# Kernel optimization log

Hardware: AMD Instinct MI355X
Metric: run time of the kernel (lower is better)

The kernel has to match this reference:

```python
import jax, jax.numpy as jnp
from jax import lax
import numpy as np

D, DI, S, K, R = 128, 256, 16, 4, 8  # d_model, d_inner, d_state, d_conv, dt_rank
B, W, N, E = 8, 64, 128, 256


def _ln(x, g, b, eps=1e-5):
    m = x.mean(-1, keepdims=True)
    v = ((x - m) ** 2).mean(-1, keepdims=True)
    return (x - m) * lax.rsqrt(v + eps) * g + b


def _mamba(x, w_in, conv_w, conv_b, w_xp, dt_w, dt_b, Alog, Dp, w_out):
    # x: (Bq, W, D) -> (Bq, W, D). Faithful mamba_ssm.Mamba math (selective scan).
    Bq, Wlen, _ = x.shape
    xz = x @ w_in                       # (Bq, W, 2*DI)
    xc, z = jnp.split(xz, 2, axis=-1)
    # causal depthwise conv over time
    xt = xc.transpose(0, 2, 1)          # (Bq, DI, W)
    xt = lax.conv_general_dilated(xt, conv_w[:, None, :], (1,), [(K - 1, 0)],
                                  feature_group_count=DI)
    xc = jax.nn.silu(xt + conv_b[None, :, None]).transpose(0, 2, 1)  # (Bq, W, DI)
    dbc = xc @ w_xp                     # (Bq, W, R+2S)
    dt = jax.nn.softplus(dbc[..., :R] @ dt_w + dt_b)   # (Bq, W, DI)
    Bm = dbc[..., R:R + S]              # (Bq, W, S)
    Cm = dbc[..., R + S:]               # (Bq, W, S)
    A = -jnp.exp(Alog)                  # (DI, S)

    def step(h, inp):
        dt_t, B_t, C_t, x_t = inp       # (Bq,DI),(Bq,S),(Bq,S),(Bq,DI)
        dA = jnp.exp(dt_t[..., None] * A)                 # (Bq,DI,S)
        h = dA * h + (dt_t * x_t)[..., None] * B_t[:, None, :]
        y = jnp.einsum('bds,bs->bd', h, C_t)
        return h, y

    h0 = jnp.zeros((Bq, DI, S), x.dtype)
    _, ys = lax.scan(step, h0, (dt.transpose(1, 0, 2), Bm.transpose(1, 0, 2),
                                Cm.transpose(1, 0, 2), xc.transpose(1, 0, 2)))
    y = ys.transpose(1, 0, 2) + xc * Dp          # D skip connection
    y = y * jax.nn.silu(z)
    return y @ w_out


def _forward(x_node, x_trace, x_log, mp_in, mp_conv_w, mp_conv_b, mp_xproj,
             mp_dt_w, mp_dt_b, mp_Alog, mp_D, mp_out, mix_w, mix_b,
             an_g, an_b, ff1_w, ff1_b, ff2_w, ff2_b, fln_g, fln_b):
    Bz, Wz, Nz, _ = x_node.shape
    Ez = x_trace.shape[2]
    # (B,W,N,D) -> (B*N, W, D) per-entity temporal sequences
    sn = x_node.transpose(0, 2, 1, 3).reshape(Bz * Nz, Wz, D)
    st = x_trace.transpose(0, 2, 1, 3).reshape(Bz * Ez, Wz, D)
    sl = x_log.transpose(0, 2, 1, 3).reshape(Bz * Nz, Wz, D)

    def mam(i, s):
        return _mamba(s, mp_in[i], mp_conv_w[i], mp_conv_b[i], mp_xproj[i],
                      mp_dt_w[i], mp_dt_b[i], mp_Alog[i], mp_D[i], mp_out[i])

    yn, yt, yl = mam(0, sn), mam(1, st), mam(2, sl)

    # cross-modal mixing of node & log with residual (dropout = identity in eval)
    cat = jnp.concatenate([yn, yl], axis=-1)          # (B*N, W, 2D)
    cat = cat + jax.nn.silu(cat @ mix_w + mix_b)
    yn, yl = jnp.split(cat, 2, axis=-1)

    # back to (B, W, N/E, D)
    yn = yn.reshape(Bz, Nz, Wz, D).transpose(0, 2, 1, 3)
    yt = yt.reshape(Bz, Ez, Wz, D).transpose(0, 2, 1, 3)
    yl = yl.reshape(Bz, Nz, Wz, D).transpose(0, 2, 1, 3)

    # AddALL: AddNorm(old, new) = LN(dropout(new) + old)
    n1 = _ln(yn + x_node, an_g[0], an_b[0])
    t1 = _ln(yt + x_trace, an_g[1], an_b[1])
    l1 = _ln(yl + x_log, an_g[2], an_b[2])

    # FFN: AddNorm(x, FeedForward(x)) per modality, LeakyReLU(0.01)
    def ffn(i, x):
        h = jax.nn.leaky_relu(x @ ff1_w[i] + ff1_b[i], 0.01)
        return _ln(h @ ff2_w[i] + ff2_b[i] + x, fln_g[i], fln_b[i])

    n2, t2, l2 = ffn(0, n1), ffn(1, t1), ffn(2, l1)
    # concat along entity axis (all feature dims = D) for a single output
    return jnp.concatenate([n2, t2, l2], axis=2)      # (B, W, 2N+E, D)


def setup_inputs() -> dict:
    key = jax.random.key(0)
    ks = jax.random.split(key, 16)
    f = lambda k, shp, s=1.0: jax.random.normal(k, shp, dtype=jnp.float32) * s
    return {
        'x_node': f(ks[0], (B, W, N, D)),
        'x_trace': f(ks[1], (B, W, E, D)),
        'x_log': f(ks[2], (B, W, N, D)),
        'mp_in': f(ks[3], (3, D, 2 * DI), 0.05),
        'mp_conv_w': f(ks[4], (3, DI, K), 0.2),
        'mp_conv_b': jnp.zeros((3, DI), jnp.float32),
        'mp_xproj': f(ks[5], (3, DI, R + 2 * S), 0.05),
        'mp_dt_w': f(ks[6], (3, R, DI), 0.1),
        'mp_dt_b': jnp.full((3, DI), float(np.log(np.expm1(0.01))), jnp.float32),
        'mp_Alog': jnp.log(jnp.broadcast_to(jnp.arange(1, S + 1, dtype=jnp.float32), (3, DI, S))),
        'mp_D': jnp.ones((3, DI), jnp.float32),
        'mp_out': f(ks[7], (3, DI, D), 0.05),
        'mix_w': f(ks[8], (2 * D, 2 * D), 0.05),
        'mix_b': jnp.zeros((2 * D,), jnp.float32),
        'an_g': jnp.ones((3, D), jnp.float32),
        'an_b': jnp.zeros((3, D), jnp.float32),
        'ff1_w': f(ks[9], (3, D, 4 * D), 0.05),
        'ff1_b': jnp.zeros((3, 4 * D), jnp.float32),
        'ff2_w': f(ks[10], (3, 4 * D, D), 0.05),
        'ff2_b': jnp.zeros((3, D), jnp.float32),
        'fln_g': jnp.ones((3, D), jnp.float32),
        'fln_b': jnp.zeros((3, D), jnp.float32),
    }


def reference(x_node, x_trace, x_log, mp_in, mp_conv_w, mp_conv_b, mp_xproj,
              mp_dt_w, mp_dt_b, mp_Alog, mp_D, mp_out, mix_w, mix_b,
              an_g, an_b, ff1_w, ff1_b, ff2_w, ff2_b, fln_g, fln_b):
    return _forward(x_node, x_trace, x_log, mp_in, mp_conv_w, mp_conv_b,
                    mp_xproj, mp_dt_w, mp_dt_b, mp_Alog, mp_D, mp_out,
                    mix_w, mix_b, an_g, an_b, ff1_w, ff1_b, ff2_w, ff2_b,
                    fln_g, fln_b)
```

## Files before the change

### kernel.cpp

```cpp
#include <hip/hip_runtime.h>
#include <hip/hip_bf16.h>

#define DEV __device__ __forceinline__

typedef __attribute__((ext_vector_type(8))) short bf16x8;
typedef __attribute__((ext_vector_type(4))) float f32x4;
typedef __attribute__((ext_vector_type(2))) float f32x2;

DEV f32x4 MF(bf16x8 a, bf16x8 b, f32x4 c) {
  return __builtin_amdgcn_mfma_f32_16x16x32_bf16(a, b, c, 0, 0, 0);
}

DEV float bf2f(unsigned short u) {
  union { unsigned int i; float f; } v; v.i = ((unsigned int)u) << 16; return v.f;
}
DEV unsigned short f2bf(float f) {
  __hip_bfloat16 h = __float2bfloat16(f);
  unsigned short r; __builtin_memcpy(&r, &h, 2); return r;
}
DEV unsigned int packbf(float a, float b) {
  float2 p; p.x = a; p.y = b;
  __hip_bfloat162 h = __float22bfloat162_rn(p);
  unsigned int r; __builtin_memcpy(&r, &h, 4); return r;
}
#define LOG2E 1.442695041f
#define LN2   0.6931471806f
DEV float silu_fast(float v) {
  float e = __builtin_amdgcn_exp2f(v * -LOG2E);
  return v * __builtin_amdgcn_rcpf(1.f + e);
}
DEV float softplus_fast(float v) {
  float e = __builtin_amdgcn_exp2f(v * LOG2E);
  float l = __builtin_amdgcn_logf(1.f + e) * LN2;
  return v > 15.f ? v : l;
}

#define WS_WINT   0
#define WS_WXPT   196608
#define WS_WOUTT  233472
#define WS_FF1T   331776
#define WS_FF2T   528384
#define WS_MIXT   724992
#define WS_TOTAL  790528

__global__ __launch_bounds__(256) void prep_kernel(
    const float* __restrict__ w_in, const float* __restrict__ w_xp,
    const float* __restrict__ w_out, const float* __restrict__ ff1,
    const float* __restrict__ ff2, const float* __restrict__ mixw,
    unsigned short* __restrict__ ws)
{
  int idx = blockIdx.x * 256 + threadIdx.x;
  if (idx >= WS_TOTAL) return;
  float v;
  if (idx < WS_WXPT) {
    int j = idx, s = j / 65536, r = j % 65536, n = r >> 7, k = r & 127;
    v = w_in[s * 65536 + k * 512 + n];
  } else if (idx < WS_WOUTT) {
    int j = idx - WS_WXPT, s = j / 12288, r = j % 12288, n = r >> 8, k = r & 255;
    v = (n < 40) ? w_xp[s * 10240 + k * 40 + n] : 0.f;
  } else if (idx < WS_FF1T) {
    int j = idx - WS_WOUTT, s = j / 32768, r = j % 32768, n = r >> 8, k = r & 255;
    v = w_out[s * 32768 + k * 128 + n];
  } else if (idx < WS_FF2T) {
    int j = idx - WS_FF1T, s = j / 65536, r = j % 65536, n = r >> 7, k = r & 127;
    v = ff1[s * 65536 + k * 512 + n];
  } else if (idx < WS_MIXT) {
    int j = idx - WS_FF2T, s = j / 65536, r = j % 65536, n = r >> 9, k = r & 511;
    v = ff2[s * 65536 + k * 128 + n];
  } else {
    int j = idx - WS_MIXT, n = j >> 8, k = j & 255;
    v = mixw[k * 256 + n];
  }
  ws[idx] = f2bf(v);
}

__global__ __launch_bounds__(256, 2) void mamba_front(
    const float* __restrict__ xn, const float* __restrict__ xt,
    const float* __restrict__ xl,
    const unsigned short* __restrict__ w_inT_all,
    const float* __restrict__ conv_w_all, const float* __restrict__ conv_b_all,
    const unsigned short* __restrict__ w_xpT_all,
    const float* __restrict__ dt_w_all, const float* __restrict__ dt_b_all,
    const float* __restrict__ Alog_all, const float* __restrict__ Dp_all,
    const unsigned short* __restrict__ w_outT_all,
    const float* __restrict__ an_g, const float* __restrict__ an_b,
    const unsigned short* __restrict__ ff1T, const float* __restrict__ fb1,
    const unsigned short* __restrict__ ff2T, const float* __restrict__ fb2,
    const float* __restrict__ fln_g, const float* __restrict__ fln_b,
    float* __restrict__ out)
{
  __shared__ __attribute__((aligned(16))) unsigned short xcz[64 * 512];
  __shared__ __attribute__((aligned(16))) char aux[16384];
  unsigned short* xs = (unsigned short*)aux;
  float* dbc = (float*)aux;

  const int tid = threadIdx.x;
  const int lane = tid & 63;
  const int wv = tid >> 6;
  const int lr = lane & 15;
  const int kg = lane >> 4;

  int blk = blockIdx.x, s, q;
  if (blk < 1024)      { s = 0; q = blk; }
  else if (blk < 3072) { s = 1; q = blk - 1024; }
  else                 { s = 2; q = blk - 3072; }
  const int SEQ = (s == 1) ? 256 : 128;
  const int slot_base = (s == 0) ? 0 : (s == 1 ? 128 : 384);
  const float* x = (s == 0) ? xn : (s == 1 ? xt : xl);
  const unsigned short* w_inT  = w_inT_all  + (size_t)s * 65536;
  const unsigned short* w_xpT  = w_xpT_all  + (size_t)s * 12288;
  const unsigned short* w_outT = w_outT_all + (size_t)s * 32768;
  const float* conv_w = conv_w_all + s * 1024;
  const float* conv_b = conv_b_all + s * 256;
  const float* dt_w   = dt_w_all + s * 2048;
  const float* dt_b   = dt_b_all + s * 256;
  const float* Alog   = Alog_all + s * 4096;
  const float* Dp     = Dp_all + s * 256;

  const int b = q / SEQ, n = q - b * SEQ;
  const float* xb = x + ((size_t)b * 64 * SEQ + n) * 128;

  for (int idx = tid; idx < 2048; idx += 256) {
    int t = idx >> 5, qd = (idx & 31) << 2;
    float4 v = *(const float4*)(xb + (size_t)t * SEQ * 128 + qd);
    uint2 p;
    p.x = packbf(v.x, v.y);
    p.y = packbf(v.z, v.w);
    *(uint2*)(&xs[t * 128 + (qd ^ ((t & 7) << 3))]) = p;
  }
  __syncthreads();

  {
    bf16x8 bx[4][4];
#pragma unroll
    for (int jt = 0; jt < 4; ++jt)
#pragma unroll
      for (int ks = 0; ks < 4; ++ks) {
        int t = jt * 16 + lr;
        bx[jt][ks] = *(const bf16x8*)(&xs[t * 128 + ((ks * 32 + kg * 8) ^ ((t & 7) << 3))]);
      }
    const int nb = wv * 128;
#pragma unroll
    for (int at = 0; at < 8; ++at) {
      bf16x8 av[4];
      int arow = nb + at * 16 + lr;
#pragma unroll
      for (int ks = 0; ks < 4; ++ks)
        av[ks] = *(const bf16x8*)(w_inT + arow * 128 + ks * 32 + kg * 8);
#pragma unroll
      for (int jt = 0; jt < 4; ++jt) {
        f32x4 c = {0.f, 0.f, 0.f, 0.f};
#pragma unroll
        for (int ks = 0; ks < 4; ++ks) c = MF(av[ks], bx[jt][ks], c);
        int t = jt * 16 + lr;
        int n0 = nb + at * 16 + kg * 4;
        uint2 p;
        p.x = packbf(c[0], c[1]);
        p.y = packbf(c[2], c[3]);
        *(uint2*)(&xcz[t * 512 + (n0 ^ ((t & 7) << 3))]) = p;
      }
    }
  }
  __syncthreads();

  {
    const int d = tid;
    float cw0 = conv_w[d * 4 + 0], cw1 = conv_w[d * 4 + 1];
    float cw2 = conv_w[d * 4 + 2], cw3 = conv_w[d * 4 + 3];
    float cb = conv_b[d];
    float xm3 = 0.f, xm2 = 0.f, xm1 = 0.f;
    for (int c0 = 0; c0 < 64; c0 += 16) {
      float xv[16];
#pragma unroll
      for (int u = 0; u < 16; ++u) {
        int t = c0 + u;
        xv[u] = bf2f(xcz[t * 512 + (d ^ ((t & 7) << 3))]);
      }
#pragma unroll
      for (int u = 0; u < 16; ++u) {
        float sv = fmaf(cw0, xm3, fmaf(cw1, xm2, fmaf(cw2, xm1, fmaf(cw3, xv[u], cb))));
        xm3 = xm2; xm2 = xm1; xm1 = xv[u];
        xv[u] = silu_fast(sv);
      }
#pragma unroll
      for (int u = 0; u < 16; ++u) {
        int t = c0 + u;
        xcz[t * 512 + (d ^ ((t & 7) << 3))] = f2bf(xv[u]);
      }
    }
  }
  __syncthreads();

  {
    bf16x8 av[8];
    int ta = wv * 16 + lr;
#pragma unroll
    for (int ks = 0; ks < 8; ++ks)
      av[ks] = *(const bf16x8*)(&xcz[ta * 512 + ((ks * 32 + kg * 8) ^ ((ta & 7) << 3))]);
#pragma unroll
    for (int ct = 0; ct < 3; ++ct) {
      f32x4 c = {0.f, 0.f, 0.f, 0.f};
#pragma unroll
      for (int ks = 0; ks < 8; ++ks) {
        bf16x8 bv = *(const bf16x8*)(w_xpT + (ct * 16 + lr) * 256 + ks * 32 + kg * 8);
        c = MF(av[ks], bv, c);
      }
      int tt = wv * 16 + kg * 4;
#pragma unroll
      for (int r = 0; r < 4; ++r)
        dbc[(tt + r) * 48 + ct * 16 + lr] = c[r];
    }
  }
  __syncthreads();

  {
    const int d = tid;
    float dtw[8];
#pragma unroll
    for (int r = 0; r < 8; ++r) dtw[r] = dt_w[r * 256 + d];
    const float dtb = dt_b[d];
    float Af2[16];
#pragma unroll
    for (int s2 = 0; s2 < 16; ++s2)
      Af2[s2] = -__builtin_amdgcn_exp2f(Alog[d * 16 + s2] * LOG2E) * LOG2E;
    const float af0l2 = Af2[0];
    bool geo = true;
#pragma unroll
    for (int s2 = 1; s2 < 16; ++s2)
      geo = geo && (fabsf(Af2[s2] - (float)(s2 + 1) * af0l2) <= 2e-4f * fabsf(Af2[s2]));
    const float Dv = Dp[d];

    const int eoff = d;
    const int zoff = 256 + d;

    if (geo) {
      f32x2 h2[8];
#pragma unroll
      for (int k = 0; k < 8; ++k) h2[k] = (f32x2){0.f, 0.f};
#pragma unroll 2
      for (int t = 0; t < 64; ++t) {
        const f32x4* dr4 = (const f32x4*)&dbc[t * 48];
        f32x4 d0 = dr4[0], d1 = dr4[1];
        float dtv = dtb;
        dtv = fmaf(dtw[0], d0[0], dtv); dtv = fmaf(dtw[1], d0[1], dtv);
        dtv = fmaf(dtw[2], d0[2], dtv); dtv = fmaf(dtw[3], d0[3], dtv);
        dtv = fmaf(dtw[4], d1[0], dtv); dtv = fmaf(dtw[5], d1[1], dtv);
        dtv = fmaf(dtw[6], d1[2], dtv); dtv = fmaf(dtw[7], d1[3], dtv);
        dtv = softplus_fast(dtv);
        int sw = (t & 7) << 3;
        int e = t * 512 + (eoff ^ sw);
        float xv = bf2f(xcz[e]);
        float zf = bf2f(xcz[t * 512 + (zoff ^ sw)]);
        float cf = dtv * xv;
        float r1 = __builtin_amdgcn_exp2f(dtv * af0l2);
        float r2 = r1 * r1;
        f32x2 r2v = {r2, r2};
        f32x2 pp = {r1, r2};
        f32x2 cf2 = {cf, cf};
        f32x2 y2 = {0.f, 0.f};
        f32x4 B0 = dr4[2], B1 = dr4[3], B2 = dr4[4], B3 = dr4[5];
        f32x4 C0 = dr4[6], C1 = dr4[7], C2 = dr4[8], C3 = dr4[9];
        f32x2 Bv[8] = {{B0[0],B0[1]},{B0[2],B0[3]},{B1[0],B1[1]},{B1[2],B1[3]},
                       {B2[0],B2[1]},{B2[2],B2[3]},{B3[0],B3[1]},{B3[2],B3[3]}};
        f32x2 Cv[8] = {{C0[0],C0[1]},{C0[2],C0[3]},{C1[0],C1[1]},{C1[2],C1[3]},
                       {C2[0],C2[1]},{C2[2],C2[3]},{C3[0],C3[1]},{C3[2],C3[3]}};
#pragma unroll
        for (int k = 0; k < 8; ++k) {
          h2[k] = __builtin_elementwise_fma(pp, h2[k], cf2 * Bv[k]);
          y2 = __builtin_elementwise_fma(h2[k], Cv[k], y2);
          pp = pp * r2v;
        }
        float y = y2[0] + y2[1];
        xcz[e] = f2bf((fmaf(xv, Dv, y)) * silu_fast(zf));
      }
    } else {
      float h[16];
#pragma unroll
      for (int s2 = 0; s2 < 16; ++s2) h[s2] = 0.f;
#pragma unroll 2
      for (int t = 0; t < 64; ++t) {
        const float* dr = &dbc[t * 48];
        float dtv = dtb;
#pragma unroll
        for (int r = 0; r < 8; ++r) dtv = fmaf(dtw[r], dr[r], dtv);
        dtv = softplus_fast(dtv);
        int sw = (t & 7) << 3;
        int e = t * 512 + (eoff ^ sw);
        float xv = bf2f(xcz[e]);
        float zf = bf2f(xcz[t * 512 + (zoff ^ sw)]);
        float cf = dtv * xv;
        float y = 0.f;
#pragma unroll
        for (int s2 = 0; s2 < 16; ++s2) {
          float dA = __builtin_amdgcn_exp2f(dtv * Af2[s2]);
          h[s2] = fmaf(dA, h[s2], cf * dr[8 + s2]);
          y = fmaf(h[s2], dr[24 + s2], y);
        }
        xcz[e] = f2bf((fmaf(xv, Dv, y)) * silu_fast(zf));
      }
    }
  }
  __syncthreads();

  {
    bf16x8 av[8];
    int ta = wv * 16 + lr;
#pragma unroll
    for (int ks = 0; ks < 8; ++ks)
      av[ks] = *(const bf16x8*)(&xcz[ta * 512 + ((ks * 32 + kg * 8) ^ ((ta & 7) << 3))]);
    f32x4 acc[8];
#pragma unroll
    for (int ct = 0; ct < 8; ++ct) {
      f32x4 c = {0.f, 0.f, 0.f, 0.f};
#pragma unroll
      for (int ks = 0; ks < 8; ++ks) {
        bf16x8 bv = *(const bf16x8*)(w_outT + (ct * 16 + lr) * 256 + ks * 32 + kg * 8);
        c = MF(av[ks], bv, c);
      }
      acc[ct] = c;
    }
    size_t ob = (size_t)b * 64 * 512 * 128 + (size_t)(slot_base + n) * 128;
    const int trow = wv * 16 + kg * 4;
    if (s != 1) {
#pragma unroll
      for (int ct = 0; ct < 8; ++ct) {
        int cc = ct * 16 + lr;
#pragma unroll
        for (int r = 0; r < 4; ++r)
          out[ob + (size_t)(trow + r) * 65536 + cc] = acc[ct][r];
      }
    } else {
      float sum[4] = {0.f, 0.f, 0.f, 0.f}, sq[4] = {0.f, 0.f, 0.f, 0.f};
#pragma unroll
      for (int ct = 0; ct < 8; ++ct) {
        int col = ct * 16 + lr;
#pragma unroll
        for (int r = 0; r < 4; ++r) {
          int t = trow + r;
          float xr = xb[(size_t)t * SEQ * 128 + col];
          float v = acc[ct][r] + xr;
          acc[ct][r] = v;
          sum[r] += v; sq[r] += v * v;
        }
      }
      float mn[4], rstd[4];
#pragma unroll
      for (int r = 0; r < 4; ++r) {
        float s1 = sum[r], s2 = sq[r];
        s1 += __shfl_xor(s1, 1); s2 += __shfl_xor(s2, 1);
        s1 += __shfl_xor(s1, 2); s2 += __shfl_xor(s2, 2);
        s1 += __shfl_xor(s1, 4); s2 += __shfl_xor(s2, 4);
        s1 += __shfl_xor(s1, 8); s2 += __shfl_xor(s2, 8);
        float mean = s1 * (1.f / 128.f);
        float var = s2 * (1.f / 128.f) - mean * mean;
        mn[r] = mean;
        rstd[r] = rsqrtf(var + 1e-5f);
      }
      const float* G  = an_g + 128;
      const float* Bv = an_b + 128;
#pragma unroll
      for (int ct = 0; ct < 8; ++ct) {
        int col = ct * 16 + lr;
        float gc = G[col], bc = Bv[col];
#pragma unroll
        for (int r = 0; r < 4; ++r) {
          int t = trow + r;
          float t1 = (acc[ct][r] - mn[r]) * rstd[r] * gc + bc;
          xs[t * 128 + (col ^ ((t & 7) << 3))] = f2bf(t1);
        }
      }
      __syncthreads();

      const unsigned short* F1 = ff1T + 65536;
      const unsigned short* F2 = ff2T + 65536;
      const float* B1 = fb1 + 512;
      const float* B2 = fb2 + 128;
      const float* FG = fln_g + 128;
      const float* FB = fln_b + 128;
      {
        bf16x8 bx[4][4];
#pragma unroll
        for (int jt = 0; jt < 4; ++jt)
#pragma unroll
          for (int ks = 0; ks < 4; ++ks) {
            int t = jt * 16 + lr;
            bx[jt][ks] = *(const bf16x8*)(&xs[t * 128 + ((ks * 32 + kg * 8) ^ ((t & 7) << 3))]);
          }
        const int nb = wv * 128;
#pragma unroll
        for (int at = 0; at < 8; ++at) {
          bf16x8 av1[4];
          int arow = nb + at * 16 + lr;
#pragma unroll
          for (int ks = 0; ks < 4; ++ks)
            av1[ks] = *(const bf16x8*)(F1 + arow * 128 + ks * 32 + kg * 8);
          float4 bias = *(const float4*)(B1 + nb + at * 16 + kg * 4);
#pragma unroll
          for (int jt = 0; jt < 4; ++jt) {
            f32x4 c = {0.f, 0.f, 0.f, 0.f};
#pragma unroll
            for (int ks = 0; ks < 4; ++ks) c = MF(av1[ks], bx[jt][ks], c);
            float v0 = c[0] + bias.x; v0 = v0 > 0.f ? v0 : 0.01f * v0;
            float v1 = c[1] + bias.y; v1 = v1 > 0.f ? v1 : 0.01f * v1;
            float v2 = c[2] + bias.z; v2 = v2 > 0.f ? v2 : 0.01f * v2;
            float v3 = c[3] + bias.w; v3 = v3 > 0.f ? v3 : 0.01f * v3;
            int t = jt * 16 + lr;
            int n0 = nb + at * 16 + kg * 4;
            uint2 p;
            p.x = packbf(v0, v1);
            p.y = packbf(v2, v3);
            *(uint2*)(&xcz[t * 512 + (n0 ^ ((t & 7) << 3))]) = p;
          }
        }
      }
      __syncthreads();
      {
        bf16x8 av2[16];
        int ta2 = wv * 16 + lr;
#pragma unroll
        for (int ks = 0; ks < 16; ++ks)
          av2[ks] = *(const bf16x8*)(&xcz[ta2 * 512 + ((ks * 32 + kg * 8) ^ ((ta2 & 7) << 3))]);
        f32x4 a2[8];
#pragma unroll
        for (int ct = 0; ct < 8; ++ct) {
          f32x4 c = {0.f, 0.f, 0.f, 0.f};
#pragma unroll
          for (int ks = 0; ks < 16; ++ks) {
            bf16x8 bv = *(const bf16x8*)(F2 + (ct * 16 + lr) * 512 + ks * 32 + kg * 8);
            c = MF(av2[ks], bv, c);
          }
          a2[ct] = c;
        }
        float vv[8][4];
        float su[4] = {0.f, 0.f, 0.f, 0.f}, sb[4] = {0.f, 0.f, 0.f, 0.f};
#pragma unroll
        for (int ct = 0; ct < 8; ++ct) {
          int col = ct * 16 + lr;
          float b2c = B2[col];
#pragma unroll
          for (int r = 0; r < 4; ++r) {
            int t = trow + r;
            float xr = bf2f(xs[t * 128 + (col ^ ((t & 7) << 3))]);
            float val = a2[ct][r] + b2c + xr;
            vv[ct][r] = val;
            su[r] += val; sb[r] += val * val;
          }
        }
        float mn2[4], rs2[4];
#pragma unroll
        for (int r = 0; r < 4; ++r) {
          float s1 = su[r], s2 = sb[r];
          s1 += __shfl_xor(s1, 1); s2 += __shfl_xor(s2, 1);
          s1 += __shfl_xor(s1, 2); s2 += __shfl_xor(s2, 2);
          s1 += __shfl_xor(s1, 4); s2 += __shfl_xor(s2, 4);
          s1 += __shfl_xor(s1, 8); s2 += __shfl_xor(s2, 8);
          float mean = s1 * (1.f / 128.f);
          float var = s2 * (1.f / 128.f) - mean * mean;
          mn2[r] = mean;
          rs2[r] = rsqrtf(var + 1e-5f);
        }
#pragma unroll
        for (int ct = 0; ct < 8; ++ct) {
          int col = ct * 16 + lr;
          float gc = FG[col], bc = FB[col];
#pragma unroll
          for (int r = 0; r < 4; ++r)
            out[ob + (size_t)(trow + r) * 65536 + col] = (vv[ct][r] - mn2[r]) * rs2[r] * gc + bc;
        }
      }
    }
  }
}

__global__ __launch_bounds__(256, 2) void mix_ffn_kernel(
    float* __restrict__ out, const unsigned short* __restrict__ mixT,
    const float* __restrict__ mix_b,
    const float* __restrict__ xn, const float* __restrict__ xl,
    const float* __restrict__ an_g, const float* __restrict__ an_b,
    const unsigned short* __restrict__ ff1T, const float* __restrict__ fb1,
    const unsigned short* __restrict__ ff2T, const float* __restrict__ fb2,
    const float* __restrict__ fln_g, const float* __restrict__ fln_b)
{
  __shared__ __attribute__((aligned(16))) unsigned short cs[64 * 256];
  __shared__ __attribute__((aligned(16))) unsigned short xs[64 * 128];
  __shared__ __attribute__((aligned(16))) unsigned short hT[64 * 256];

  const int tid = threadIdx.x;
  const int lane = tid & 63;
  const int wv = tid >> 6;
  const int lr = lane & 15;
  const int kg = lane >> 4;
  const int bn = blockIdx.x;
  const int b = bn >> 7, n = bn & 127;
  const size_t base_n = (((size_t)b * 64) * 512 + n) * 128;
  const size_t base_l = (((size_t)b * 64) * 512 + 384 + n) * 128;

  for (int idx = tid; idx < 4096; idx += 256) {
    int t = idx >> 6, r = idx & 63;
    int half = r >> 5, qd = (r & 31) << 2;
    const float* src = out + (half ? base_l : base_n) + (size_t)t * 65536 + qd;
    float4 v = *(const float4*)src;
    int col = half * 128 + qd;
    uint2 p;
    p.x = packbf(v.x, v.y);
    p.y = packbf(v.z, v.w);
    *(uint2*)(&cs[t * 256 + (col ^ ((t & 7) << 3))]) = p;
  }
  __syncthreads();

  bf16x8 av[8];
  int ta = wv * 16 + lr;
#pragma unroll
  for (int ks = 0; ks < 8; ++ks)
    av[ks] = *(const bf16x8*)(&cs[ta * 256 + ((ks * 32 + kg * 8) ^ ((ta & 7) << 3))]);

  const int trow = wv * 16 + kg * 4;
#pragma unroll
  for (int half = 0; half < 2; ++half) {
    const int sf = half ? 2 : 0;
    const float* xres_base = half ? xl : xn;
    f32x4 acc[8];
#pragma unroll
// ... 146 lines not shown
        s1 += __shfl_xor(s1, 8); s2 += __shfl_xor(s2, 8);
        float mean = s1 * (1.f / 128.f);
        float var = s2 * (1.f / 128.f) - mean * mean;
        mn2[r] = mean;
        rs2[r] = rsqrtf(var + 1e-5f);
      }
      size_t base = half ? base_l : base_n;
#pragma unroll
      for (int ct = 0; ct < 8; ++ct) {
        int col = ct * 16 + lr;
        float gc = FG[col], bc = FB[col];
#pragma unroll
        for (int r = 0; r < 4; ++r)
          out[base + (size_t)(trow + r) * 65536 + col] = (vv[ct][r] - mn2[r]) * rs2[r] * gc + bc;
      }
    }
    __syncthreads();
  }
}

extern "C" void kernel_launch(void* const* d_in, const int* in_sizes, int n_in,
                              void* d_out, int out_size, void* d_ws, size_t ws_size,
                              hipStream_t stream) {
  (void)in_sizes; (void)n_in; (void)out_size; (void)ws_size;
  const float* x_node  = (const float*)d_in[0];
  const float* x_trace = (const float*)d_in[1];
  const float* x_log   = (const float*)d_in[2];
  const float* mp_in     = (const float*)d_in[3];
  const float* mp_conv_w = (const float*)d_in[4];
  const float* mp_conv_b = (const float*)d_in[5];
  const float* mp_xproj  = (const float*)d_in[6];
  const float* mp_dt_w   = (const float*)d_in[7];
  const float* mp_dt_b   = (const float*)d_in[8];
  const float* mp_Alog   = (const float*)d_in[9];
  const float* mp_D      = (const float*)d_in[10];
  const float* mp_out    = (const float*)d_in[11];
  const float* mix_w = (const float*)d_in[12];
  const float* mix_b = (const float*)d_in[13];
  const float* an_g  = (const float*)d_in[14];
  const float* an_b  = (const float*)d_in[15];
  const float* ff1_w = (const float*)d_in[16];
  const float* ff1_b = (const float*)d_in[17];
  const float* ff2_w = (const float*)d_in[18];
  const float* ff2_b = (const float*)d_in[19];
  const float* fln_g = (const float*)d_in[20];
  const float* fln_b = (const float*)d_in[21];
  float* out = (float*)d_out;

  unsigned short* ws = (unsigned short*)d_ws;

  prep_kernel<<<(WS_TOTAL + 255) / 256, 256, 0, stream>>>(
      mp_in, mp_xproj, mp_out, ff1_w, ff2_w, mix_w, ws);

  mamba_front<<<4096, 256, 0, stream>>>(
      x_node, x_trace, x_log,
      ws + WS_WINT, mp_conv_w, mp_conv_b, ws + WS_WXPT,
      mp_dt_w, mp_dt_b, mp_Alog, mp_D, ws + WS_WOUTT,
      an_g, an_b,
      ws + WS_FF1T, ff1_b, ws + WS_FF2T, ff2_b, fln_g, fln_b,
      out);

  mix_ffn_kernel<<<1024, 256, 0, stream>>>(
      out, ws + WS_MIXT, mix_b, x_node, x_log, an_g, an_b,
      ws + WS_FF1T, ff1_b, ws + WS_FF2T, ff2_b, fln_g, fln_b);
}
```

Before: 792.9 us.

## Split trace FFN into separate kernel and widen mamba_front to 512 threads

Doubles the mamba_front block to 512 threads and splits the in_proj, conv, x_proj, silu(z) gating and out_proj stages across both halves. The selective scan still runs on 256 threads while the other 256 apply silu to z in parallel. The trace-stream feed-forward block (ff1, ff2, layernorm) moves out of mamba_front into a new ffn_trace kernel that reads the intermediate result back from global memory. This cuts per-block register and LDS pressure and the imbalance between stream types, at the cost of an extra kernel launch, an extra global round trip, and idle threads during the scan.

```diff
diff --git a/kernel.cpp b/kernel.cpp
--- a/kernel.cpp
+++ b/kernel.cpp
@@ -74,7 +74,7 @@
   ws[idx] = f2bf(v);
 }
 
-__global__ __launch_bounds__(256, 2) void mamba_front(
+__global__ __launch_bounds__(512, 4) void mamba_front(
     const float* __restrict__ xn, const float* __restrict__ xt,
     const float* __restrict__ xl,
     const unsigned short* __restrict__ w_inT_all,
@@ -84,9 +84,6 @@
     const float* __restrict__ Alog_all, const float* __restrict__ Dp_all,
     const unsigned short* __restrict__ w_outT_all,
     const float* __restrict__ an_g, const float* __restrict__ an_b,
-    const unsigned short* __restrict__ ff1T, const float* __restrict__ fb1,
-    const unsigned short* __restrict__ ff2T, const float* __restrict__ fb2,
-    const float* __restrict__ fln_g, const float* __restrict__ fln_b,
     float* __restrict__ out)
 {
   __shared__ __attribute__((aligned(16))) unsigned short xcz[64 * 512];
@@ -120,7 +117,7 @@
   const int b = q / SEQ, n = q - b * SEQ;
   const float* xb = x + ((size_t)b * 64 * SEQ + n) * 128;
 
-  for (int idx = tid; idx < 2048; idx += 256) {
+  for (int idx = tid; idx < 2048; idx += 512) {
     int t = idx >> 5, qd = (idx & 31) << 2;
     float4 v = *(const float4*)(xb + (size_t)t * SEQ * 128 + qd);
     uint2 p;
@@ -139,9 +136,9 @@
         int t = jt * 16 + lr;
         bx[jt][ks] = *(const bf16x8*)(&xs[t * 128 + ((ks * 32 + kg * 8) ^ ((t & 7) << 3))]);
       }
-    const int nb = wv * 128;
-#pragma unroll
-    for (int at = 0; at < 8; ++at) {
+    const int nb = wv * 64;
+#pragma unroll
+    for (int at = 0; at < 4; ++at) {
       bf16x8 av[4];
       int arow = nb + at * 16 + lr;
 #pragma unroll
@@ -164,12 +161,19 @@
   __syncthreads();
 
   {
-    const int d = tid;
+    const int d = tid & 255;
+    const int hf = tid >> 8;
     float cw0 = conv_w[d * 4 + 0], cw1 = conv_w[d * 4 + 1];
     float cw2 = conv_w[d * 4 + 2], cw3 = conv_w[d * 4 + 3];
     float cb = conv_b[d];
     float xm3 = 0.f, xm2 = 0.f, xm1 = 0.f;
-    for (int c0 = 0; c0 < 64; c0 += 16) {
+    if (hf) {
+      xm3 = bf2f(xcz[29 * 512 + (d ^ ((29 & 7) << 3))]);
+      xm2 = bf2f(xcz[30 * 512 + (d ^ ((30 & 7) << 3))]);
+      xm1 = bf2f(xcz[31 * 512 + (d ^ ((31 & 7) << 3))]);
+    }
+    __syncthreads();
+    for (int c0 = hf * 32; c0 < hf * 32 + 32; c0 += 16) {
       float xv[16];
 #pragma unroll
       for (int u = 0; u < 16; ++u) {
@@ -192,20 +196,35 @@
   __syncthreads();
 
   {
+    const int tta = (wv < 4) ? wv : (wv - 4);
     bf16x8 av[8];
-    int ta = wv * 16 + lr;
+    int ta = tta * 16 + lr;
 #pragma unroll
     for (int ks = 0; ks < 8; ++ks)
       av[ks] = *(const bf16x8*)(&xcz[ta * 512 + ((ks * 32 + kg * 8) ^ ((ta & 7) << 3))]);
-#pragma unroll
-    for (int ct = 0; ct < 3; ++ct) {
+    int tt = tta * 16 + kg * 4;
+    if (wv < 4) {
+#pragma unroll
+      for (int cc = 0; cc < 2; ++cc) {
+        int ct = cc * 2;
+        f32x4 c = {0.f, 0.f, 0.f, 0.f};
+#pragma unroll
+        for (int ks = 0; ks < 8; ++ks) {
+          bf16x8 bv = *(const bf16x8*)(w_xpT + (ct * 16 + lr) * 256 + ks * 32 + kg * 8);
+          c = MF(av[ks], bv, c);
+        }
+#pragma unroll
+        for (int r = 0; r < 4; ++r)
+          dbc[(tt + r) * 48 + ct * 16 + lr] = c[r];
+      }
+    } else {
+      const int ct = 1;
       f32x4 c = {0.f, 0.f, 0.f, 0.f};
 #pragma unroll
       for (int ks = 0; ks < 8; ++ks) {
         bf16x8 bv = *(const bf16x8*)(w_xpT + (ct * 16 + lr) * 256 + ks * 32 + kg * 8);
         c = MF(av[ks], bv, c);
       }
-      int tt = wv * 16 + kg * 4;
 #pragma unroll
       for (int r = 0; r < 4; ++r)
         dbc[(tt + r) * 48 + ct * 16 + lr] = c[r];
@@ -213,7 +232,7 @@
   }
   __syncthreads();
 
-  {
+  if (tid < 256) {
     const int d = tid;
     float dtw[8];
 #pragma unroll
@@ -229,9 +248,6 @@
     for (int s2 = 1; s2 < 16; ++s2)
       geo = geo && (fabsf(Af2[s2] - (float)(s2 + 1) * af0l2) <= 2e-4f * fabsf(Af2[s2]));
     const float Dv = Dp[d];
-
-    const int eoff = d;
-    const int zoff = 256 + d;
 
     if (geo) {
       f32x2 h2[8];
@@ -247,10 +263,8 @@
         dtv = fmaf(dtw[4], d1[0], dtv); dtv = fmaf(dtw[5], d1[1], dtv);
         dtv = fmaf(dtw[6], d1[2], dtv); dtv = fmaf(dtw[7], d1[3], dtv);
         dtv = softplus_fast(dtv);
-        int sw = (t & 7) << 3;
-        int e = t * 512 + (eoff ^ sw);
+        int e = t * 512 + (d ^ ((t & 7) << 3));
         float xv = bf2f(xcz[e]);
-        float zf = bf2f(xcz[t * 512 + (zoff ^ sw)]);
         float cf = dtv * xv;
         float r1 = __builtin_amdgcn_exp2f(dtv * af0l2);
         float r2 = r1 * r1;
@@ -271,7 +285,7 @@
           pp = pp * r2v;
         }
         float y = y2[0] + y2[1];
-        xcz[e] = f2bf((fmaf(xv, Dv, y)) * silu_fast(zf));
+        xcz[e] = f2bf(fmaf(xv, Dv, y));
       }
     } else {
       float h[16];
@@ -284,10 +298,8 @@
 #pragma unroll
         for (int r = 0; r < 8; ++r) dtv = fmaf(dtw[r], dr[r], dtv);
         dtv = softplus_fast(dtv);
-        int sw = (t & 7) << 3;
-        int e = t * 512 + (eoff ^ sw);
+        int e = t * 512 + (d ^ ((t & 7) << 3));
         float xv = bf2f(xcz[e]);
-        float zf = bf2f(xcz[t * 512 + (zoff ^ sw)]);
         float cf = dtv * xv;
         float y = 0.f;
 #pragma unroll
@@ -296,13 +308,57 @@
           h[s2] = fmaf(dA, h[s2], cf * dr[8 + s2]);
           y = fmaf(h[s2], dr[24 + s2], y);
         }
-        xcz[e] = f2bf((fmaf(xv, Dv, y)) * silu_fast(zf));
-      }
+        xcz[e] = f2bf(fmaf(xv, Dv, y));
+      }
+    }
+  } else {
+    const int d2 = tid - 256;
+#pragma unroll 4
+    for (int t = 0; t < 64; ++t) {
+      int ez = t * 512 + ((256 + d2) ^ ((t & 7) << 3));
+      xcz[ez] = f2bf(silu_fast(bf2f(xcz[ez])));
     }
   }
   __syncthreads();
 
   {
+    const int d = tid & 255;
+    const int hf = tid >> 8;
+#pragma unroll 4
+    for (int t = hf * 32; t < hf * 32 + 32; ++t) {
+      int sw = (t & 7) << 3;
+      int e = t * 512 + (d ^ sw);
+      int ez = t * 512 + ((256 + d) ^ sw);
+      xcz[e] = f2bf(bf2f(xcz[e]) * bf2f(xcz[ez]));
+    }
+  }
+  __syncthreads();
+
+  size_t ob = (size_t)b * 64 * 512 * 128 + (size_t)(slot_base + n) * 128;
+  if (s != 1) {
+    const int tta = wv & 3;
+    const int cb = (wv >> 2) * 4;
+    bf16x8 av[8];
+    int ta = tta * 16 + lr;
+#pragma unroll
+    for (int ks = 0; ks < 8; ++ks)
+      av[ks] = *(const bf16x8*)(&xcz[ta * 512 + ((ks * 32 + kg * 8) ^ ((ta & 7) << 3))]);
+    const int trow = tta * 16 + kg * 4;
+#pragma unroll
+    for (int c2 = 0; c2 < 4; ++c2) {
+      int ct = cb + c2;
+      f32x4 c = {0.f, 0.f, 0.f, 0.f};
+#pragma unroll
+      for (int ks = 0; ks < 8; ++ks) {
+        bf16x8 bv = *(const bf16x8*)(w_outT + (ct * 16 + lr) * 256 + ks * 32 + kg * 8);
+        c = MF(av[ks], bv, c);
+      }
+      int cc = ct * 16 + lr;
+#pragma unroll
+      for (int r = 0; r < 4; ++r)
+        out[ob + (size_t)(trow + r) * 65536 + cc] = c[r];
+    }
+  } else if (wv < 4) {
     bf16x8 av[8];
     int ta = wv * 16 + lr;
 #pragma unroll
@@ -319,155 +375,170 @@
       }
       acc[ct] = c;
     }
-    size_t ob = (size_t)b * 64 * 512 * 128 + (size_t)(slot_base + n) * 128;
     const int trow = wv * 16 + kg * 4;
-    if (s != 1) {
-#pragma unroll
-      for (int ct = 0; ct < 8; ++ct) {
-        int cc = ct * 16 + lr;
-#pragma unroll
-        for (int r = 0; r < 4; ++r)
-          out[ob + (size_t)(trow + r) * 65536 + cc] = acc[ct][r];
-      }
-    } else {
-      float sum[4] = {0.f, 0.f, 0.f, 0.f}, sq[4] = {0.f, 0.f, 0.f, 0.f};
-#pragma unroll
-      for (int ct = 0; ct < 8; ++ct) {
-        int col = ct * 16 + lr;
-#pragma unroll
-        for (int r = 0; r < 4; ++r) {
-          int t = trow + r;
-          float xr = xb[(size_t)t * SEQ * 128 + col];
-          float v = acc[ct][r] + xr;
-          acc[ct][r] = v;
-          sum[r] += v; sq[r] += v * v;
-        }
-      }
-      float mn[4], rstd[4];
+    float sum[4] = {0.f, 0.f, 0.f, 0.f}, sq[4] = {0.f, 0.f, 0.f, 0.f};
+#pragma unroll
+    for (int ct = 0; ct < 8; ++ct) {
+      int col = ct * 16 + lr;
 #pragma unroll
       for (int r = 0; r < 4; ++r) {
-        float s1 = sum[r], s2 = sq[r];
-        s1 += __shfl_xor(s1, 1); s2 += __shfl_xor(s2, 1);
-        s1 += __shfl_xor(s1, 2); s2 += __shfl_xor(s2, 2);
-        s1 += __shfl_xor(s1, 4); s2 += __shfl_xor(s2, 4);
-        s1 += __shfl_xor(s1, 8); s2 += __shfl_xor(s2, 8);
-        float mean = s1 * (1.f / 128.f);
-        float var = s2 * (1.f / 128.f) - mean * mean;
-        mn[r] = mean;
-        rstd[r] = rsqrtf(var + 1e-5f);
-      }
-      const float* G  = an_g + 128;
-      const float* Bv = an_b + 128;
-#pragma unroll
-      for (int ct = 0; ct < 8; ++ct) {
-        int col = ct * 16 + lr;
-        float gc = G[col], bc = Bv[col];
-#pragma unroll
-        for (int r = 0; r < 4; ++r) {
-          int t = trow + r;
-          float t1 = (acc[ct][r] - mn[r]) * rstd[r] * gc + bc;
-          xs[t * 128 + (col ^ ((t & 7) << 3))] = f2bf(t1);
-        }
-      }
-      __syncthreads();
-
-      const unsigned short* F1 = ff1T + 65536;
-      const unsigned short* F2 = ff2T + 65536;
-      const float* B1 = fb1 + 512;
-      const float* B2 = fb2 + 128;
-      const float* FG = fln_g + 128;
-      const float* FB = fln_b + 128;
-      {
-        bf16x8 bx[4][4];
-#pragma unroll
-        for (int jt = 0; jt < 4; ++jt)
-#pragma unroll
-          for (int ks = 0; ks < 4; ++ks) {
-            int t = jt * 16 + lr;
-            bx[jt][ks] = *(const bf16x8*)(&xs[t * 128 + ((ks * 32 + kg * 8) ^ ((t & 7) << 3))]);
-          }
-        const int nb = wv * 128;
-#pragma unroll
-        for (int at = 0; at < 8; ++at) {
-          bf16x8 av1[4];
-          int arow = nb + at * 16 + lr;
-#pragma unroll
-          for (int ks = 0; ks < 4; ++ks)
-            av1[ks] = *(const bf16x8*)(F1 + arow * 128 + ks * 32 + kg * 8);
-          float4 bias = *(const float4*)(B1 + nb + at * 16 + kg * 4);
-#pragma unroll
-          for (int jt = 0; jt < 4; ++jt) {
-            f32x4 c = {0.f, 0.f, 0.f, 0.f};
-#pragma unroll
-            for (int ks = 0; ks < 4; ++ks) c = MF(av1[ks], bx[jt][ks], c);
-            float v0 = c[0] + bias.x; v0 = v0 > 0.f ? v0 : 0.01f * v0;
-            float v1 = c[1] + bias.y; v1 = v1 > 0.f ? v1 : 0.01f * v1;
-            float v2 = c[2] + bias.z; v2 = v2 > 0.f ? v2 : 0.01f * v2;
-            float v3 = c[3] + bias.w; v3 = v3 > 0.f ? v3 : 0.01f * v3;
-            int t = jt * 16 + lr;
-            int n0 = nb + at * 16 + kg * 4;
-            uint2 p;
-            p.x = packbf(v0, v1);
-            p.y = packbf(v2, v3);
-            *(uint2*)(&xcz[t * 512 + (n0 ^ ((t & 7) << 3))]) = p;
-          }
-        }
-      }
-      __syncthreads();
-      {
-        bf16x8 av2[16];
-        int ta2 = wv * 16 + lr;
-#pragma unroll
-        for (int ks = 0; ks < 16; ++ks)
-          av2[ks] = *(const bf16x8*)(&xcz[ta2 * 512 + ((ks * 32 + kg * 8) ^ ((ta2 & 7) << 3))]);
-        f32x4 a2[8];
-#pragma unroll
-        for (int ct = 0; ct < 8; ++ct) {
-          f32x4 c = {0.f, 0.f, 0.f, 0.f};
-#pragma unroll
-          for (int ks = 0; ks < 16; ++ks) {
-            bf16x8 bv = *(const bf16x8*)(F2 + (ct * 16 + lr) * 512 + ks * 32 + kg * 8);
-            c = MF(av2[ks], bv, c);
-          }
-          a2[ct] = c;
-        }
-        float vv[8][4];
-        float su[4] = {0.f, 0.f, 0.f, 0.f}, sb[4] = {0.f, 0.f, 0.f, 0.f};
-#pragma unroll
-        for (int ct = 0; ct < 8; ++ct) {
-          int col = ct * 16 + lr;
-          float b2c = B2[col];
-#pragma unroll
-          for (int r = 0; r < 4; ++r) {
-            int t = trow + r;
-            float xr = bf2f(xs[t * 128 + (col ^ ((t & 7) << 3))]);
-            float val = a2[ct][r] + b2c + xr;
-            vv[ct][r] = val;
-            su[r] += val; sb[r] += val * val;
-          }
-        }
-        float mn2[4], rs2[4];
-#pragma unroll
-        for (int r = 0; r < 4; ++r) {
-          float s1 = su[r], s2 = sb[r];
-          s1 += __shfl_xor(s1, 1); s2 += __shfl_xor(s2, 1);
-          s1 += __shfl_xor(s1, 2); s2 += __shfl_xor(s2, 2);
-          s1 += __shfl_xor(s1, 4); s2 += __shfl_xor(s2, 4);
-          s1 += __shfl_xor(s1, 8); s2 += __shfl_xor(s2, 8);
-          float mean = s1 * (1.f / 128.f);
-          float var = s2 * (1.f / 128.f) - mean * mean;
-          mn2[r] = mean;
-          rs2[r] = rsqrtf(var + 1e-5f);
-        }
-#pragma unroll
-        for (int ct = 0; ct < 8; ++ct) {
-          int col = ct * 16 + lr;
-          float gc = FG[col], bc = FB[col];
-#pragma unroll
-          for (int r = 0; r < 4; ++r)
-            out[ob + (size_t)(trow + r) * 65536 + col] = (vv[ct][r] - mn2[r]) * rs2[r] * gc + bc;
-        }
-      }
+        int t = trow + r;
+        float xr = xb[(size_t)t * SEQ * 128 + col];
+        float v = acc[ct][r] + xr;
+        acc[ct][r] = v;
+        sum[r] += v; sq[r] += v * v;
+      }
+    }
+    float mn[4], rstd[4];
+#pragma unroll
+    for (int r = 0; r < 4; ++r) {
+      float s1 = sum[r], s2 = sq[r];
+      s1 += __shfl_xor(s1, 1); s2 += __shfl_xor(s2, 1);
+      s1 += __shfl_xor(s1, 2); s2 += __shfl_xor(s2, 2);
+      s1 += __shfl_xor(s1, 4); s2 += __shfl_xor(s2, 4);
+      s1 += __shfl_xor(s1, 8); s2 += __shfl_xor(s2, 8);
+      float mean = s1 * (1.f / 128.f);
+      float var = s2 * (1.f / 128.f) - mean * mean;
+      mn[r] = mean;
+      rstd[r] = rsqrtf(var + 1e-5f);
+    }
+    const float* G  = an_g + 128;
+    const float* Bv = an_b + 128;
+#pragma unroll
+    for (int ct = 0; ct < 8; ++ct) {
+      int col = ct * 16 + lr;
+      float gc = G[col], bc = Bv[col];
+#pragma unroll
+      for (int r = 0; r < 4; ++r)
+        out[ob + (size_t)(trow + r) * 65536 + col] = (acc[ct][r] - mn[r]) * rstd[r] * gc + bc;
+    }
+  }
+}
+
+__global__ __launch_bounds__(256, 2) void ffn_trace(
+    float* __restrict__ out,
+    const unsigned short* __restrict__ ff1T, const float* __restrict__ b1,
+    const unsigned short* __restrict__ ff2T, const float* __restrict__ b2,
+    const float* __restrict__ g, const float* __restrict__ bb)
+{
+  __shared__ __attribute__((aligned(16))) unsigned short hT[64 * 512];
+  __shared__ __attribute__((aligned(16))) unsigned short xs[64 * 128];
+
+  const int tid = threadIdx.x;
+  const int lane = tid & 63;
+  const int wv = tid >> 6;
+  const int lr = lane & 15;
+  const int kg = lane >> 4;
+  const int tok0 = (blockIdx.x >> 2) * 512 + 128 + (blockIdx.x & 3) * 64;
+  const unsigned short* F1 = ff1T + 65536;
+  const unsigned short* F2 = ff2T + 65536;
+  const float* B1 = b1 + 512;
+  const float* B2 = b2 + 128;
+  const float* G = g + 128;
+  const float* Bb = bb + 128;
+
+  for (int idx = tid; idx < 2048; idx += 256) {
+    int t = idx >> 5, qd = (idx & 31) << 2;
+    float4 v = *(const float4*)(out + (size_t)(tok0 + t) * 128 + qd);
+    uint2 p;
+    p.x = packbf(v.x, v.y);
+    p.y = packbf(v.z, v.w);
+    *(uint2*)(&xs[t * 128 + (qd ^ ((t & 7) << 3))]) = p;
+  }
+  __syncthreads();
+
+  {
+    bf16x8 bx[4][4];
+#pragma unroll
+    for (int jt = 0; jt < 4; ++jt)
+#pragma unroll
+      for (int ks = 0; ks < 4; ++ks) {
+        int t = jt * 16 + lr;
+        bx[jt][ks] = *(const bf16x8*)(&xs[t * 128 + ((ks * 32 + kg * 8) ^ ((t & 7) << 3))]);
+      }
+    const int nb = wv * 128;
+#pragma unroll
+    for (int at = 0; at < 8; ++at) {
+      bf16x8 av[4];
+      int arow = nb + at * 16 + lr;
+#pragma unroll
+      for (int ks = 0; ks < 4; ++ks)
+        av[ks] = *(const bf16x8*)(F1 + arow * 128 + ks * 32 + kg * 8);
+      float4 bias = *(const float4*)(B1 + nb + at * 16 + kg * 4);
+#pragma unroll
+      for (int jt = 0; jt < 4; ++jt) {
+        f32x4 c = {0.f, 0.f, 0.f, 0.f};
+#pragma unroll
+        for (int ks = 0; ks < 4; ++ks) c = MF(av[ks], bx[jt][ks], c);
+        float v0 = c[0] + bias.x; v0 = v0 > 0.f ? v0 : 0.01f * v0;
+        float v1 = c[1] + bias.y; v1 = v1 > 0.f ? v1 : 0.01f * v1;
+        float v2 = c[2] + bias.z; v2 = v2 > 0.f ? v2 : 0.01f * v2;
+        float v3 = c[3] + bias.w; v3 = v3 > 0.f ? v3 : 0.01f * v3;
+        int t = jt * 16 + lr;
+        int n0 = nb + at * 16 + kg * 4;
+        uint2 p;
+        p.x = packbf(v0, v1);
+        p.y = packbf(v2, v3);
+        *(uint2*)(&hT[t * 512 + (n0 ^ ((t & 7) << 3))]) = p;
+      }
+    }
+  }
+  __syncthreads();
+
+  {
+    bf16x8 av[16];
+    int ta = wv * 16 + lr;
+#pragma unroll
+    for (int ks = 0; ks < 16; ++ks)
+      av[ks] = *(const bf16x8*)(&hT[ta * 512 + ((ks * 32 + kg * 8) ^ ((ta & 7) << 3))]);
+    f32x4 acc[8];
+#pragma unroll
+    for (int ct = 0; ct < 8; ++ct) {
+      f32x4 c = {0.f, 0.f, 0.f, 0.f};
+#pragma unroll
+      for (int ks = 0; ks < 16; ++ks) {
+        bf16x8 bv = *(const bf16x8*)(F2 + (ct * 16 + lr) * 512 + ks * 32 + kg * 8);
+        c = MF(av[ks], bv, c);
+      }
+      acc[ct] = c;
+    }
+
+    float v[8][4];
+    float sum[4] = {0.f, 0.f, 0.f, 0.f}, sq[4] = {0.f, 0.f, 0.f, 0.f};
+    const int trow = wv * 16 + kg * 4;
+#pragma unroll
+    for (int ct = 0; ct < 8; ++ct) {
+      int col = ct * 16 + lr;
+      float b2c = B2[col];
+#pragma unroll
+      for (int r = 0; r < 4; ++r) {
+        int t = trow + r;
+        float xr = bf2f(xs[t * 128 + (col ^ ((t & 7) << 3))]);
+        float val = acc[ct][r] + b2c + xr;
+        v[ct][r] = val;
+        sum[r] += val; sq[r] += val * val;
+      }
+    }
+    float mn[4], rstd[4];
+#pragma unroll
+    for (int r = 0; r < 4; ++r) {
+      float s1 = sum[r], s2 = sq[r];
+      s1 += __shfl_xor(s1, 1); s2 += __shfl_xor(s2, 1);
+      s1 += __shfl_xor(s1, 2); s2 += __shfl_xor(s2, 2);
+      s1 += __shfl_xor(s1, 4); s2 += __shfl_xor(s2, 4);
+      s1 += __shfl_xor(s1, 8); s2 += __shfl_xor(s2, 8);
+      float mean = s1 * (1.f / 128.f);
+      float var = s2 * (1.f / 128.f) - mean * mean;
+      mn[r] = mean;
+      rstd[r] = rsqrtf(var + 1e-5f);
+    }
+#pragma unroll
+    for (int ct = 0; ct < 8; ++ct) {
+      int col = ct * 16 + lr;
+      float gc = G[col], bc = Bb[col];
+#pragma unroll
+      for (int r = 0; r < 4; ++r)
+        out[(size_t)(tok0 + trow + r) * 128 + col] = (v[ct][r] - mn[r]) * rstd[r] * gc + bc;
     }
   }
 }
@@ -720,13 +791,14 @@
   prep_kernel<<<(WS_TOTAL + 255) / 256, 256, 0, stream>>>(
       mp_in, mp_xproj, mp_out, ff1_w, ff2_w, mix_w, ws);
 
-  mamba_front<<<4096, 256, 0, stream>>>(
+  mamba_front<<<4096, 512, 0, stream>>>(
       x_node, x_trace, x_log,
       ws + WS_WINT, mp_conv_w, mp_conv_b, ws + WS_WXPT,
       mp_dt_w, mp_dt_b, mp_Alog, mp_D, ws + WS_WOUTT,
-      an_g, an_b,
-      ws + WS_FF1T, ff1_b, ws + WS_FF2T, ff2_b, fln_g, fln_b,
-      out);
+      an_g, an_b, out);
+
+  ffn_trace<<<2048, 256, 0, stream>>>(
+      out, ws + WS_FF1T, ff1_b, ws + WS_FF2T, ff2_b, fln_g, fln_b);
 
   mix_ffn_kernel<<<1024, 256, 0, stream>>>(
       out, ws + WS_MIXT, mix_b, x_node, x_log, an_g, an_b,
```

Result: slower. 874.2 us (+10.2%).

## Split trace-branch FFN out of mamba_front into a separate kernel

Applied to the files above, without the earlier changes.

Removes the feed-forward block and final layernorm for the trace stream from the mamba_front kernel. mamba_front now writes the post-attention layernorm result directly to the output buffer. A new ffn_trace kernel reloads it, runs the two MFMA GEMMs with the residual and layernorm, and writes back. This likely aims to lower register and LDS pressure in the heavy scan kernel, at the cost of an extra global round trip and a kernel launch.

```diff
diff --git a/kernel.cpp b/kernel.cpp
--- a/kernel.cpp
+++ b/kernel.cpp
@@ -84,9 +84,6 @@
     const float* __restrict__ Alog_all, const float* __restrict__ Dp_all,
     const unsigned short* __restrict__ w_outT_all,
     const float* __restrict__ an_g, const float* __restrict__ an_b,
-    const unsigned short* __restrict__ ff1T, const float* __restrict__ fb1,
-    const unsigned short* __restrict__ ff2T, const float* __restrict__ fb2,
-    const float* __restrict__ fln_g, const float* __restrict__ fln_b,
     float* __restrict__ out)
 {
   __shared__ __attribute__((aligned(16))) unsigned short xcz[64 * 512];
@@ -363,111 +360,137 @@
         int col = ct * 16 + lr;
         float gc = G[col], bc = Bv[col];
 #pragma unroll
-        for (int r = 0; r < 4; ++r) {
-          int t = trow + r;
-          float t1 = (acc[ct][r] - mn[r]) * rstd[r] * gc + bc;
-          xs[t * 128 + (col ^ ((t & 7) << 3))] = f2bf(t1);
-        }
-      }
-      __syncthreads();
-
-      const unsigned short* F1 = ff1T + 65536;
-      const unsigned short* F2 = ff2T + 65536;
-      const float* B1 = fb1 + 512;
-      const float* B2 = fb2 + 128;
-      const float* FG = fln_g + 128;
-      const float* FB = fln_b + 128;
-      {
-        bf16x8 bx[4][4];
-#pragma unroll
-        for (int jt = 0; jt < 4; ++jt)
-#pragma unroll
-          for (int ks = 0; ks < 4; ++ks) {
-            int t = jt * 16 + lr;
-            bx[jt][ks] = *(const bf16x8*)(&xs[t * 128 + ((ks * 32 + kg * 8) ^ ((t & 7) << 3))]);
-          }
-        const int nb = wv * 128;
-#pragma unroll
-        for (int at = 0; at < 8; ++at) {
-          bf16x8 av1[4];
-          int arow = nb + at * 16 + lr;
-#pragma unroll
-          for (int ks = 0; ks < 4; ++ks)
-            av1[ks] = *(const bf16x8*)(F1 + arow * 128 + ks * 32 + kg * 8);
-          float4 bias = *(const float4*)(B1 + nb + at * 16 + kg * 4);
-#pragma unroll
-          for (int jt = 0; jt < 4; ++jt) {
-            f32x4 c = {0.f, 0.f, 0.f, 0.f};
-#pragma unroll
-            for (int ks = 0; ks < 4; ++ks) c = MF(av1[ks], bx[jt][ks], c);
-            float v0 = c[0] + bias.x; v0 = v0 > 0.f ? v0 : 0.01f * v0;
-            float v1 = c[1] + bias.y; v1 = v1 > 0.f ? v1 : 0.01f * v1;
-            float v2 = c[2] + bias.z; v2 = v2 > 0.f ? v2 : 0.01f * v2;
-            float v3 = c[3] + bias.w; v3 = v3 > 0.f ? v3 : 0.01f * v3;
-            int t = jt * 16 + lr;
-            int n0 = nb + at * 16 + kg * 4;
-            uint2 p;
-            p.x = packbf(v0, v1);
-            p.y = packbf(v2, v3);
-            *(uint2*)(&xcz[t * 512 + (n0 ^ ((t & 7) << 3))]) = p;
-          }
-        }
-      }
-      __syncthreads();
-      {
-        bf16x8 av2[16];
-        int ta2 = wv * 16 + lr;
-#pragma unroll
-        for (int ks = 0; ks < 16; ++ks)
-          av2[ks] = *(const bf16x8*)(&xcz[ta2 * 512 + ((ks * 32 + kg * 8) ^ ((ta2 & 7) << 3))]);
-        f32x4 a2[8];
-#pragma unroll
-        for (int ct = 0; ct < 8; ++ct) {
-          f32x4 c = {0.f, 0.f, 0.f, 0.f};
-#pragma unroll
-          for (int ks = 0; ks < 16; ++ks) {
-            bf16x8 bv = *(const bf16x8*)(F2 + (ct * 16 + lr) * 512 + ks * 32 + kg * 8);
-            c = MF(av2[ks], bv, c);
-          }
-          a2[ct] = c;
-        }
-        float vv[8][4];
-        float su[4] = {0.f, 0.f, 0.f, 0.f}, sb[4] = {0.f, 0.f, 0.f, 0.f};
-#pragma unroll
-        for (int ct = 0; ct < 8; ++ct) {
-          int col = ct * 16 + lr;
-          float b2c = B2[col];
-#pragma unroll
-          for (int r = 0; r < 4; ++r) {
-            int t = trow + r;
-            float xr = bf2f(xs[t * 128 + (col ^ ((t & 7) << 3))]);
-            float val = a2[ct][r] + b2c + xr;
-            vv[ct][r] = val;
-            su[r] += val; sb[r] += val * val;
-          }
-        }
-        float mn2[4], rs2[4];
-#pragma unroll
-        for (int r = 0; r < 4; ++r) {
-          float s1 = su[r], s2 = sb[r];
-          s1 += __shfl_xor(s1, 1); s2 += __shfl_xor(s2, 1);
-          s1 += __shfl_xor(s1, 2); s2 += __shfl_xor(s2, 2);
-          s1 += __shfl_xor(s1, 4); s2 += __shfl_xor(s2, 4);
-          s1 += __shfl_xor(s1, 8); s2 += __shfl_xor(s2, 8);
-          float mean = s1 * (1.f / 128.f);
-          float var = s2 * (1.f / 128.f) - mean * mean;
-          mn2[r] = mean;
-          rs2[r] = rsqrtf(var + 1e-5f);
-        }
-#pragma unroll
-        for (int ct = 0; ct < 8; ++ct) {
-          int col = ct * 16 + lr;
-          float gc = FG[col], bc = FB[col];
-#pragma unroll
-          for (int r = 0; r < 4; ++r)
-            out[ob + (size_t)(trow + r) * 65536 + col] = (vv[ct][r] - mn2[r]) * rs2[r] * gc + bc;
-        }
-      }
+        for (int r = 0; r < 4; ++r)
+          out[ob + (size_t)(trow + r) * 65536 + col] = (acc[ct][r] - mn[r]) * rstd[r] * gc + bc;
+      }
+    }
+  }
+}
+
+__global__ __launch_bounds__(256, 2) void ffn_trace(
+    float* __restrict__ out,
+    const unsigned short* __restrict__ ff1T, const float* __restrict__ b1,
+    const unsigned short* __restrict__ ff2T, const float* __restrict__ b2,
+    const float* __restrict__ g, const float* __restrict__ bb)
+{
+  __shared__ __attribute__((aligned(16))) unsigned short hT[64 * 512];
+  __shared__ __attribute__((aligned(16))) unsigned short xs[64 * 128];
+
+  const int tid = threadIdx.x;
+  const int lane = tid & 63;
+  const int wv = tid >> 6;
+  const int lr = lane & 15;
+  const int kg = lane >> 4;
+  const int tok0 = (blockIdx.x >> 2) * 512 + 128 + (blockIdx.x & 3) * 64;
+  const unsigned short* F1 = ff1T + 65536;
+  const unsigned short* F2 = ff2T + 65536;
+  const float* B1 = b1 + 512;
+  const float* B2 = b2 + 128;
+  const float* G = g + 128;
+  const float* Bb = bb + 128;
+
+  for (int idx = tid; idx < 2048; idx += 256) {
+    int t = idx >> 5, qd = (idx & 31) << 2;
+    float4 v = *(const float4*)(out + (size_t)(tok0 + t) * 128 + qd);
+    uint2 p;
+    p.x = packbf(v.x, v.y);
+    p.y = packbf(v.z, v.w);
+    *(uint2*)(&xs[t * 128 + (qd ^ ((t & 7) << 3))]) = p;
+  }
+  __syncthreads();
+
+  {
+    bf16x8 bx[4][4];
+#pragma unroll
+    for (int jt = 0; jt < 4; ++jt)
+#pragma unroll
+      for (int ks = 0; ks < 4; ++ks) {
+        int t = jt * 16 + lr;
+        bx[jt][ks] = *(const bf16x8*)(&xs[t * 128 + ((ks * 32 + kg * 8) ^ ((t & 7) << 3))]);
+      }
+    const int nb = wv * 128;
+#pragma unroll
+    for (int at = 0; at < 8; ++at) {
+      bf16x8 av[4];
+      int arow = nb + at * 16 + lr;
+#pragma unroll
+      for (int ks = 0; ks < 4; ++ks)
+        av[ks] = *(const bf16x8*)(F1 + arow * 128 + ks * 32 + kg * 8);
+      float4 bias = *(const float4*)(B1 + nb + at * 16 + kg * 4);
+#pragma unroll
+      for (int jt = 0; jt < 4; ++jt) {
+        f32x4 c = {0.f, 0.f, 0.f, 0.f};
+#pragma unroll
+        for (int ks = 0; ks < 4; ++ks) c = MF(av[ks], bx[jt][ks], c);
+        float v0 = c[0] + bias.x; v0 = v0 > 0.f ? v0 : 0.01f * v0;
+        float v1 = c[1] + bias.y; v1 = v1 > 0.f ? v1 : 0.01f * v1;
+        float v2 = c[2] + bias.z; v2 = v2 > 0.f ? v2 : 0.01f * v2;
+        float v3 = c[3] + bias.w; v3 = v3 > 0.f ? v3 : 0.01f * v3;
+        int t = jt * 16 + lr;
+        int n0 = nb + at * 16 + kg * 4;
+        uint2 p;
+        p.x = packbf(v0, v1);
+        p.y = packbf(v2, v3);
+        *(uint2*)(&hT[t * 512 + (n0 ^ ((t & 7) << 3))]) = p;
+      }
+    }
+  }
+  __syncthreads();
+
+  {
+    bf16x8 av[16];
+    int ta = wv * 16 + lr;
+#pragma unroll
+    for (int ks = 0; ks < 16; ++ks)
+      av[ks] = *(const bf16x8*)(&hT[ta * 512 + ((ks * 32 + kg * 8) ^ ((ta & 7) << 3))]);
+    f32x4 acc[8];
+#pragma unroll
+    for (int ct = 0; ct < 8; ++ct) {
+      f32x4 c = {0.f, 0.f, 0.f, 0.f};
+#pragma unroll
+      for (int ks = 0; ks < 16; ++ks) {
+        bf16x8 bv = *(const bf16x8*)(F2 + (ct * 16 + lr) * 512 + ks * 32 + kg * 8);
+        c = MF(av[ks], bv, c);
+      }
+      acc[ct] = c;
+    }
+
+    float v[8][4];
+    float sum[4] = {0.f, 0.f, 0.f, 0.f}, sq[4] = {0.f, 0.f, 0.f, 0.f};
+    const int trow = wv * 16 + kg * 4;
+#pragma unroll
+    for (int ct = 0; ct < 8; ++ct) {
+      int col = ct * 16 + lr;
+      float b2c = B2[col];
+#pragma unroll
+      for (int r = 0; r < 4; ++r) {
+        int t = trow + r;
+        float xr = bf2f(xs[t * 128 + (col ^ ((t & 7) << 3))]);
+        float val = acc[ct][r] + b2c + xr;
+        v[ct][r] = val;
+        sum[r] += val; sq[r] += val * val;
+      }
+    }
+    float mn[4], rstd[4];
+#pragma unroll
+    for (int r = 0; r < 4; ++r) {
+      float s1 = sum[r], s2 = sq[r];
+      s1 += __shfl_xor(s1, 1); s2 += __shfl_xor(s2, 1);
+      s1 += __shfl_xor(s1, 2); s2 += __shfl_xor(s2, 2);
+      s1 += __shfl_xor(s1, 4); s2 += __shfl_xor(s2, 4);
+      s1 += __shfl_xor(s1, 8); s2 += __shfl_xor(s2, 8);
+      float mean = s1 * (1.f / 128.f);
+      float var = s2 * (1.f / 128.f) - mean * mean;
+      mn[r] = mean;
+      rstd[r] = rsqrtf(var + 1e-5f);
+    }
+#pragma unroll
+    for (int ct = 0; ct < 8; ++ct) {
+      int col = ct * 16 + lr;
+      float gc = G[col], bc = Bb[col];
+#pragma unroll
+      for (int r = 0; r < 4; ++r)
+        out[(size_t)(tok0 + trow + r) * 128 + col] = (v[ct][r] - mn[r]) * rstd[r] * gc + bc;
     }
   }
 }
@@ -724,9 +747,10 @@
       x_node, x_trace, x_log,
       ws + WS_WINT, mp_conv_w, mp_conv_b, ws + WS_WXPT,
       mp_dt_w, mp_dt_b, mp_Alog, mp_D, ws + WS_WOUTT,
-      an_g, an_b,
-      ws + WS_FF1T, ff1_b, ws + WS_FF2T, ff2_b, fln_g, fln_b,
-      out);
+      an_g, an_b, out);
+
+  ffn_trace<<<2048, 256, 0, stream>>>(
+      out, ws + WS_FF1T, ff1_b, ws + WS_FF2T, ff2_b, fln_g, fln_b);
 
   mix_ffn_kernel<<<1024, 256, 0, stream>>>(
       out, ws + WS_MIXT, mix_b, x_node, x_log, an_g, an_b,
```

Measured after the change: 858.5 us. +8.3%, slower.
